# Kernel optimization log

Hardware: AMD Instinct MI355X
Metric: run time of the kernel (lower is better)

Reference implementation:

```python
import jax, jax.numpy as jnp
import numpy as np

B, S, D, F, E = 4, 2048, 512, 2048, 8


def setup_inputs() -> dict:
    key = jax.random.key(0)
    ks = jax.random.split(key, 8)
    s1 = 1.0 / np.sqrt(D)
    s2 = 1.0 / np.sqrt(F)
    return {
        "hidden_states": jax.random.normal(ks[0], (B, S, D), jnp.float32),
        "gating_probs": jax.random.uniform(ks[1], (B, S, E), jnp.float32),
        "shared_gate_prob": jax.random.uniform(ks[2], (B, S, 1), jnp.float32),
        "W1": jax.random.normal(ks[3], (E, D, F), jnp.float32) * s1,
        "b1": jnp.zeros((E, F), jnp.float32),
        "W2": jax.random.normal(ks[4], (E, F, D), jnp.float32) * s2,
        "b2": jnp.zeros((E, D), jnp.float32),
        "Ws1": jax.random.normal(ks[5], (D, F), jnp.float32) * s1,
        "bs1": jnp.zeros((F,), jnp.float32),
        "Ws2": jax.random.normal(ks[6], (F, D), jnp.float32) * s2,
        "bs2": jnp.zeros((D,), jnp.float32),
    }


def reference(hidden_states, gating_probs, shared_gate_prob,
              W1, b1, W2, b2, Ws1, bs1, Ws2, bs2):
    # Dense evaluation of ALL experts over all tokens (faithful to the source).
    # h: [B, E, S, F]
    h = jax.nn.gelu(jnp.einsum("bsd,edf->besf", hidden_states, W1) + b1[None, :, None, :])
    # y: [B, E, S, D]
    y = jnp.einsum("besf,efd->besd", h, W2) + b2[None, :, None, :]
    # weighted_sum combine with per-token gating probs: [B, S, D]
    expert_output = jnp.einsum("besd,bse->bsd", y, gating_probs)
    # shared expert
    hs = jax.nn.gelu(hidden_states @ Ws1 + bs1)
    shared_out = hs @ Ws2 + bs2
    return (1.0 - shared_gate_prob) * expert_output + shared_gate_prob * shared_out
```

## Files before the change

### kernel.cpp

```cpp
#include <hip/hip_runtime.h>

#define Dm 512
#define Fm 2048
#define Mm 8192
#define KTOT 18432

typedef __attribute__((ext_vector_type(8))) short short8;
typedef __attribute__((ext_vector_type(4))) float f32x4;


__device__ __forceinline__ unsigned short f2bf(float f) {
  unsigned u = __builtin_bit_cast(unsigned, f);
  u = (u + 0x7FFFu + ((u >> 16) & 1u)) >> 16;
  return (unsigned short)u;
}

__device__ __forceinline__ float fast_exp2(float x) {
  float r; asm("v_exp_f32 %0, %1" : "=v"(r) : "v"(x)); return r;
}
__device__ __forceinline__ float fast_rcp(float x) {
  float r; asm("v_rcp_f32 %0, %1" : "=v"(r) : "v"(x)); return r;
}

__device__ __forceinline__ void gload_lds16(const void* g, void* lp) {
  __builtin_amdgcn_global_load_lds(
      (const __attribute__((address_space(1))) void*)(unsigned long long)(g),
      (__attribute__((address_space(3))) void*)(unsigned)(unsigned long long)(lp),
      16, 0, 0);
}

__device__ __forceinline__ f32x4 mfma16(short8 a, short8 b, f32x4 c) {
  asm("v_mfma_f32_16x16x32_bf16 %0, %1, %2, %0" : "+v"(c) : "v"(a), "v"(b));
  return c;
}

#define WAIT_BARRIER(n) asm volatile("s_waitcnt vmcnt(" #n ")\n\ts_barrier" ::: "memory")


__global__ void cvtx_k(const float* __restrict__ src, unsigned short* __restrict__ dst, int n) {
  int i = (blockIdx.x * 256 + threadIdx.x) * 4;
  if (i >= n) return;
  const float4 v = *(const float4*)(src + i);
  unsigned a = (unsigned)f2bf(v.x) | ((unsigned)f2bf(v.y) << 16);
  unsigned b = (unsigned)f2bf(v.z) | ((unsigned)f2bf(v.w) << 16);
  uint2 o; o.x = a; o.y = b;
  *(uint2*)(dst + i) = o;
}

__global__ void wts_k(const float* __restrict__ gp, const float* __restrict__ sg,
                      float* __restrict__ wts) {
  int t = blockIdx.x * 256 + threadIdx.x;
  if (t >= Mm) return;
  float s = sg[t];
  float om = 1.0f - s;
#pragma unroll
  for (int e = 0; e < 8; ++e) wts[t * 9 + e] = om * gp[t * 8 + e];
  wts[t * 9 + 8] = s;
}

__global__ void wt_k(const float* __restrict__ W1, const float* __restrict__ Ws1,
                     const float* __restrict__ W2, const float* __restrict__ Ws2,
                     unsigned short* __restrict__ W1T, unsigned short* __restrict__ W2T) {
  __shared__ float tile[32][33];
  const int tx = threadIdx.x, ty = threadIdx.y;
  int bid = blockIdx.x;
  if (bid < 9216) {
    const int e = bid >> 10;
    const int rem = bid & 1023;
    const float* src = (e < 8) ? (W1 + (size_t)e * Dm * Fm) : Ws1;
    const int c0 = (rem & 63) << 5;
    const int r0 = (rem >> 6) << 5;
#pragma unroll
    for (int j = ty; j < 32; j += 8) tile[j][tx] = src[(size_t)(r0 + j) * Fm + c0 + tx];
    __syncthreads();
    unsigned short* de = W1T + (size_t)e * Fm * Dm;
#pragma unroll
    for (int j = ty; j < 32; j += 8) de[(size_t)(c0 + j) * Dm + r0 + tx] = f2bf(tile[tx][j]);
  } else {
    bid -= 9216;
    const int e = bid >> 10;
    const int rem = bid & 1023;
    const float* src = (e < 8) ? (W2 + (size_t)e * Fm * Dm) : Ws2;
    const int c0 = (rem & 15) << 5;
    const int r0 = (rem >> 4) << 5;
#pragma unroll
    for (int j = ty; j < 32; j += 8) tile[j][tx] = src[(size_t)(r0 + j) * Dm + c0 + tx];
    __syncthreads();
#pragma unroll
    for (int j = ty; j < 32; j += 8)
      W2T[(size_t)(c0 + j) * KTOT + (size_t)e * Fm + r0 + tx] = f2bf(tile[tx][j]);
  }
}


__global__ __launch_bounds__(256)
void gemm1_k(const unsigned short* __restrict__ Xb,
             const unsigned short* __restrict__ W1T,
             const float* __restrict__ b1, const float* __restrict__ bs1,
             const float* __restrict__ wts,
             unsigned short* __restrict__ Hs,
             int gbase, int Gg, int ldH) {
  __shared__ __attribute__((aligned(16))) unsigned short As[2][128 * 64];
  __shared__ __attribute__((aligned(16))) unsigned short Bs[2][128 * 64];

  const int tid = threadIdx.x, l = tid & 63, w = tid >> 6;
  const int wr = w >> 1, wc = w & 1;
  const int nwg = Gg << 10;
  const int wg = (blockIdx.x & 7) * (nwg >> 3) + (blockIdx.x >> 3);
  const int el = wg >> 10;
  const int rem = wg & 1023;
  const int grp = rem >> 7;
  const int sub = rem & 127;
  const int tn = (sub & 15) << 7;
  const int tm = ((grp << 3) + (sub >> 4)) << 7;
  const int eg = gbase + el;
  const unsigned short* BT = W1T + (size_t)eg * Fm * Dm;
  const float* bias = (eg < 8) ? (b1 + (size_t)eg * Fm) : bs1;

  f32x4 acc[4][4];
  const f32x4 zz = {0.f, 0.f, 0.f, 0.f};
#pragma unroll
  for (int mi = 0; mi < 4; ++mi)
#pragma unroll
    for (int ni = 0; ni < 4; ++ni) acc[mi][ni] = zz;

  const int srow = tid >> 3;
  const int sc = ((tid & 7) ^ (srow & 7)) << 3;

#define BPERM1(r) (((r) & 64) | (((r) & 15) << 2) | (((r) >> 4) & 3))

#define STAGE1(buf, ks)                                                          \
  {                                                                              \
    _Pragma("unroll")                                                            \
    for (int i = 0; i < 4; ++i) {                                                \
      const int row = i * 32 + srow;                                             \
      gload_lds16(Xb + (size_t)(tm + row) * Dm + (ks) + sc,                      \
                  (char*)As[buf] + i * 4096 + tid * 16);                         \
      gload_lds16(BT + (size_t)(tn + BPERM1(row)) * Dm + (ks) + sc,              \
                  (char*)Bs[buf] + i * 4096 + tid * 16);                         \
    }                                                                            \
  }

  STAGE1(0, 0);
  __syncthreads();

  for (int t = 0; t < 8; ++t) {
    const int cur = t & 1;
    if (t < 7) STAGE1(cur ^ 1, (t + 1) << 6);
#pragma unroll
    for (int kk = 0; kk < 2; ++kk) {
      const int kbx = (kk * 64 + ((l >> 4) << 4)) ^ ((l & 7) << 4);
      short8 af[4], bfr[4];
#pragma unroll
      for (int mi = 0; mi < 4; ++mi)
        af[mi] = *(const short8*)((const char*)As[cur] + ((wr * 64 + mi * 16 + (l & 15)) << 7) + kbx);
#pragma unroll
      for (int ni = 0; ni < 4; ++ni)
        bfr[ni] = *(const short8*)((const char*)Bs[cur] + ((wc * 64 + ni * 16 + (l & 15)) << 7) + kbx);
#pragma unroll
      for (int mi = 0; mi < 4; ++mi)
#pragma unroll
        for (int ni = 0; ni < 4; ++ni)
          acc[mi][ni] = mfma16(af[mi], bfr[ni], acc[mi][ni]);
    }
    if (t < 7) __syncthreads();
  }
#undef STAGE1
#undef BPERM1

  const int row0 = tm + wr * 64 + ((l >> 4) << 2);
  const int col0 = tn + wc * 64 + ((l & 15) << 2);
  const size_t hb = (size_t)el * Fm;
  const float4 bv = *(const float4*)(bias + col0);

  const float Ac = -2.3022120f;
  const float Bc = -0.10294341f;

#pragma unroll
  for (int mi = 0; mi < 4; ++mi) {
#pragma unroll
    for (int r = 0; r < 4; ++r) {
      const int rr = row0 + mi * 16 + r;
      const float wt = wts[(size_t)rr * 9 + eg];
      float g[4];
      const float bvv[4] = {bv.x, bv.y, bv.z, bv.w};
#pragma unroll
      for (int ni = 0; ni < 4; ++ni) {
        const float v = acc[mi][ni][r] + bvv[ni];
        const float t2 = v * fmaf(Bc, v * v, Ac);
        g[ni] = wt * v * fast_rcp(1.0f + fast_exp2(t2));
      }
      uint2 pk;
      asm("v_cvt_pk_bf16_f32 %0, %1, %2" : "=v"(pk.x) : "v"(g[0]), "v"(g[1]));
      asm("v_cvt_pk_bf16_f32 %0, %1, %2" : "=v"(pk.y) : "v"(g[2]), "v"(g[3]));
      *(uint2*)(Hs + (size_t)rr * ldH + hb + col0) = pk;
    }
  }
}


__global__ __launch_bounds__(256)
void gemm2_k(const unsigned short* __restrict__ A, int lda,
             const unsigned short* __restrict__ BT, int ldb,
             float* __restrict__ out,
             const float* __restrict__ wts,
             const float* __restrict__ b2, const float* __restrict__ bs2,
             int Kt, int g0) {
  __shared__ __attribute__((aligned(16))) unsigned short As[3][128 * 64];
  __shared__ __attribute__((aligned(16))) unsigned short Bs[3][64 * 64];

  const int tid = threadIdx.x, l = tid & 63, w = tid >> 6;
  const int wr = w >> 1, wc = w & 1;
  const int wg = (blockIdx.x & 7) * 64 + (blockIdx.x >> 3);
  const int gm = wg >> 6;
  const int sub = wg & 63;
  const int tn = (sub & 7) << 6;
  const int tm = ((gm << 3) + (sub >> 3)) << 7;

  f32x4 acc[4][2];
  const f32x4 zz = {0.f, 0.f, 0.f, 0.f};
#pragma unroll
  for (int mi = 0; mi < 4; ++mi)
#pragma unroll
    for (int ni = 0; ni < 2; ++ni) acc[mi][ni] = zz;

  const int srow = tid >> 3;
  const int sc = ((tid & 7) ^ (srow & 7)) << 3;

#define BPERM2(r) (((r) & 32) | (((r) & 15) << 1) | (((r) >> 4) & 1))

#define STAGE2(buf, ks)                                                          \
  {                                                                              \
    _Pragma("unroll")                                                            \
    for (int i = 0; i < 4; ++i) {                                                \
      const int row = i * 32 + srow;                                             \
      gload_lds16(A + (size_t)(tm + row) * lda + (ks) + sc,                      \
                  (char*)As[buf] + i * 4096 + tid * 16);                         \
    }                                                                            \
    _Pragma("unroll")                                                            \
    for (int i = 0; i < 2; ++i) {                                                \
      const int row = i * 32 + srow;                                             \
      gload_lds16(BT + (size_t)(tn + BPERM2(row)) * ldb + (ks) + sc,             \
                  (char*)Bs[buf] + i * 4096 + tid * 16);                         \
    }                                                                            \
  }

  const int NT = Kt >> 6;
  STAGE2(0, 0);
  STAGE2(1, 64);

#pragma unroll 1
  for (int t = 0; t < NT; ++t) {
    const int cur = t % 3;
    if (t + 1 < NT) { WAIT_BARRIER(6); }
    else            { WAIT_BARRIER(0); }
    __builtin_amdgcn_sched_barrier(0);
    if (t + 2 < NT) {
      const int nb = (t + 2) % 3;
      STAGE2(nb, (t + 2) << 6);
    }
#pragma unroll
    for (int kk = 0; kk < 2; ++kk) {
      const int kbx = (kk * 64 + ((l >> 4) << 4)) ^ ((l & 7) << 4);
      short8 af[4], bfr[2];
#pragma unroll
      for (int mi = 0; mi < 4; ++mi)
        af[mi] = *(const short8*)((const char*)As[cur] + ((wr * 64 + mi * 16 + (l & 15)) << 7) + kbx);
#pragma unroll
      for (int ni = 0; ni < 2; ++ni)
        bfr[ni] = *(const short8*)((const char*)Bs[cur] + ((wc * 32 + ni * 16 + (l & 15)) << 7) + kbx);
#pragma unroll
      for (int mi = 0; mi < 4; ++mi)
#pragma unroll
        for (int ni = 0; ni < 2; ++ni)
          acc[mi][ni] = mfma16(af[mi], bfr[ni], acc[mi][ni]);
    }
  }
#undef STAGE2
#undef BPERM2

  const int row0 = tm + wr * 64 + ((l >> 4) << 2);
  const int col0 = tn + wc * 32 + ((l & 15) << 1);

  if (g0) {
    float bcol[2][9];
#pragma unroll
    for (int ni = 0; ni < 2; ++ni) {
      const int c = col0 + ni;
#pragma unroll
      for (int e = 0; e < 8; ++e) bcol[ni][e] = b2[(e << 9) + c];
      bcol[ni][8] = bs2[c];
    }
#pragma unroll
    for (int mi = 0; mi < 4; ++mi)
#pragma unroll
      for (int r = 0; r < 4; ++r) {
        const int rr = row0 + mi * 16 + r;
        const float* wrow = wts + (size_t)rr * 9;
        float b0 = 0.f, b1v = 0.f;
#pragma unroll
        for (int e = 0; e < 9; ++e) { b0 += wrow[e] * bcol[0][e]; b1v += wrow[e] * bcol[1][e]; }
        float2 o;
        o.x = acc[mi][0][r] + b0;
        o.y = acc[mi][1][r] + b1v;
        *(float2*)(out + (size_t)rr * Dm + col0) = o;
      }
  } else {
#pragma unroll
    for (int mi = 0; mi < 4; ++mi)
#pragma unroll
      for (int r = 0; r < 4; ++r) {
        float* p = out + (size_t)(row0 + mi * 16 + r) * Dm + col0;
        float2 o = *(float2*)p;
        o.x += acc[mi][0][r];
        o.y += acc[mi][1][r];
        *(float2*)p = o;
      }
  }
}


extern "C" void kernel_launch(void* const* d_in, const int* in_sizes, int n_in,
                              void* d_out, int out_size, void* d_ws, size_t ws_size,
                              hipStream_t stream) {
  const float* x   = (const float*)d_in[0];
  const float* gp  = (const float*)d_in[1];
  const float* sg  = (const float*)d_in[2];
  const float* W1  = (const float*)d_in[3];
  const float* b1  = (const float*)d_in[4];
  const float* W2  = (const float*)d_in[5];
  const float* b2  = (const float*)d_in[6];
  const float* Ws1 = (const float*)d_in[7];
  const float* bs1 = (const float*)d_in[8];
  const float* Ws2 = (const float*)d_in[9];
  const float* bs2 = (const float*)d_in[10];
  float* out = (float*)d_out;

  const size_t szXb  = (size_t)Mm * Dm * 2;
  const size_t szWts = (size_t)Mm * 9 * 4;
  const size_t szW1T = (size_t)9 * Fm * Dm * 2;
  const size_t szW2T = (size_t)9 * Fm * Dm * 2;
  const size_t base  = szXb + szWts + szW1T + szW2T;

  int G;
  if      (ws_size >= base + (size_t)Mm * 9 * Fm * 2) G = 9;
  else if (ws_size >= base + (size_t)Mm * 3 * Fm * 2) G = 3;
  else if (ws_size >= base + (size_t)Mm * 2 * Fm * 2) G = 2;
  else if (ws_size >= base + (size_t)Mm * 1 * Fm * 2) G = 1;
  else return;

  char* ws = (char*)d_ws;
  unsigned short* Xb  = (unsigned short*)(ws);
  float*          wts = (float*)(ws + szXb);
  unsigned short* W1T = (unsigned short*)(ws + szXb + szWts);
  unsigned short* W2T = (unsigned short*)(ws + szXb + szWts + szW1T);
  unsigned short* Hs  = (unsigned short*)(ws + base);
  const int ldH = G * Fm;

  cvtx_k<<<dim3((Mm * Dm) / 1024), dim3(256), 0, stream>>>(x, Xb, Mm * Dm);
  wts_k<<<dim3(Mm / 256), dim3(256), 0, stream>>>(gp, sg, wts);
  wt_k<<<dim3(2 * 9 * 1024), dim3(32, 8), 0, stream>>>(W1, Ws1, W2, Ws2, W1T, W2T);

  for (int gb = 0; gb < 9; gb += G) {
    const int Gg = (9 - gb < G) ? (9 - gb) : G;
    gemm1_k<<<dim3(Gg * 1024), dim3(256), 0, stream>>>(
        Xb, W1T, b1, bs1, wts, Hs, gb, Gg, ldH);
    gemm2_k<<<dim3(512), dim3(256), 0, stream>>>(
        Hs, ldH, W2T + (size_t)gb * Fm, KTOT, out, wts, b2, bs2, Gg * Fm, gb == 0 ? 1 : 0);
  }
}
```

Baseline: 422.0 us.

## Make gemm1 persistent with 128x64 tiles and a triple-buffered continuous pipeline

gemm1 now launches a fixed 512 workgroups. Each one walks a sequence of 128x64 output tiles and keeps a three-stage LDS pipeline running across tile boundaries, using vmcnt-based waits in place of full syncthreads. Gating weights are written in an expert-major copy so the epilogue can read them as vectors. The aim is to hide load latency and remove per-tile launch and drain costs, at the price of smaller tiles that reuse less data and an extra workspace buffer.

```diff
diff --git a/kernel.cpp b/kernel.cpp
--- a/kernel.cpp
+++ b/kernel.cpp
@@ -35,6 +35,8 @@
 }
 
 #define WAIT_BARRIER(n) asm volatile("s_waitcnt vmcnt(" #n ")\n\ts_barrier" ::: "memory")
+
+#define BPERM2(r) (((r) & 32) | (((r) & 15) << 1) | (((r) >> 4) & 1))
 
 
 __global__ void cvtx_k(const float* __restrict__ src, unsigned short* __restrict__ dst, int n) {
@@ -48,14 +50,19 @@
 }
 
 __global__ void wts_k(const float* __restrict__ gp, const float* __restrict__ sg,
-                      float* __restrict__ wts) {
+                      float* __restrict__ wts, float* __restrict__ wtsE) {
   int t = blockIdx.x * 256 + threadIdx.x;
   if (t >= Mm) return;
   float s = sg[t];
   float om = 1.0f - s;
 #pragma unroll
-  for (int e = 0; e < 8; ++e) wts[t * 9 + e] = om * gp[t * 8 + e];
+  for (int e = 0; e < 8; ++e) {
+    float v = om * gp[t * 8 + e];
+    wts[t * 9 + e] = v;
+    wtsE[(size_t)e * Mm + t] = v;
+  }
   wts[t * 9 + 8] = s;
+  wtsE[(size_t)8 * Mm + t] = s;
 }
 
 __global__ void wt_k(const float* __restrict__ W1, const float* __restrict__ Ws1,
@@ -97,105 +104,130 @@
 void gemm1_k(const unsigned short* __restrict__ Xb,
              const unsigned short* __restrict__ W1T,
              const float* __restrict__ b1, const float* __restrict__ bs1,
-             const float* __restrict__ wts,
+             const float* __restrict__ wtsE,
              unsigned short* __restrict__ Hs,
              int gbase, int Gg, int ldH) {
-  __shared__ __attribute__((aligned(16))) unsigned short As[2][128 * 64];
-  __shared__ __attribute__((aligned(16))) unsigned short Bs[2][128 * 64];
+  __shared__ __attribute__((aligned(16))) unsigned short As[3][128 * 64];
+  __shared__ __attribute__((aligned(16))) unsigned short Bs[3][64 * 64];
 
   const int tid = threadIdx.x, l = tid & 63, w = tid >> 6;
   const int wr = w >> 1, wc = w & 1;
-  const int nwg = Gg << 10;
-  const int wg = (blockIdx.x & 7) * (nwg >> 3) + (blockIdx.x >> 3);
-  const int el = wg >> 10;
-  const int rem = wg & 1023;
-  const int grp = rem >> 7;
-  const int sub = rem & 127;
-  const int tn = (sub & 15) << 7;
-  const int tm = ((grp << 3) + (sub >> 4)) << 7;
-  const int eg = gbase + el;
-  const unsigned short* BT = W1T + (size_t)eg * Fm * Dm;
-  const float* bias = (eg < 8) ? (b1 + (size_t)eg * Fm) : bs1;
-
-  f32x4 acc[4][4];
+  const int TPB = Gg << 2;
+  const int NS = TPB << 3;
+  const int cbase = ((blockIdx.x & 7) * 64 + (blockIdx.x >> 3)) * TPB;
+
+  f32x4 acc[4][2];
   const f32x4 zz = {0.f, 0.f, 0.f, 0.f};
 #pragma unroll
   for (int mi = 0; mi < 4; ++mi)
 #pragma unroll
-    for (int ni = 0; ni < 4; ++ni) acc[mi][ni] = zz;
+    for (int ni = 0; ni < 2; ++ni) acc[mi][ni] = zz;
 
   const int srow = tid >> 3;
   const int sc = ((tid & 7) ^ (srow & 7)) << 3;
 
-#define BPERM1(r) (((r) & 64) | (((r) & 15) << 2) | (((r) >> 4) & 3))
-
-#define STAGE1(buf, ks)                                                          \
+#define STAGEP(buf, s2)                                                          \
   {                                                                              \
+    const int T_ = cbase + ((s2) >> 3);                                          \
+    const int e_ = T_ >> 11;                                                     \
+    const int rem_ = T_ & 2047;                                                  \
+    const int tn_ = (rem_ & 31) << 6;                                            \
+    const int tm_ = (rem_ >> 5) << 7;                                            \
+    const int ks_ = ((s2) & 7) << 6;                                             \
+    const unsigned short* BT_ = W1T + (size_t)(gbase + e_) * (Fm * Dm);          \
     _Pragma("unroll")                                                            \
     for (int i = 0; i < 4; ++i) {                                                \
       const int row = i * 32 + srow;                                             \
-      gload_lds16(Xb + (size_t)(tm + row) * Dm + (ks) + sc,                      \
+      gload_lds16(Xb + (size_t)(tm_ + row) * Dm + ks_ + sc,                      \
                   (char*)As[buf] + i * 4096 + tid * 16);                         \
-      gload_lds16(BT + (size_t)(tn + BPERM1(row)) * Dm + (ks) + sc,              \
+    }                                                                            \
+    _Pragma("unroll")                                                            \
+    for (int i = 0; i < 2; ++i) {                                                \
+      const int row = i * 32 + srow;                                             \
+      gload_lds16(BT_ + (size_t)(tn_ + BPERM2(row)) * Dm + ks_ + sc,             \
                   (char*)Bs[buf] + i * 4096 + tid * 16);                         \
     }                                                                            \
   }
 
-  STAGE1(0, 0);
-  __syncthreads();
-
-  for (int t = 0; t < 8; ++t) {
-    const int cur = t & 1;
-    if (t < 7) STAGE1(cur ^ 1, (t + 1) << 6);
-#pragma unroll
-    for (int kk = 0; kk < 2; ++kk) {
-      const int kbx = (kk * 64 + ((l >> 4) << 4)) ^ ((l & 7) << 4);
-      short8 af[4], bfr[4];
-#pragma unroll
-      for (int mi = 0; mi < 4; ++mi)
-        af[mi] = *(const short8*)((const char*)As[cur] + ((wr * 64 + mi * 16 + (l & 15)) << 7) + kbx);
-#pragma unroll
-      for (int ni = 0; ni < 4; ++ni)
-        bfr[ni] = *(const short8*)((const char*)Bs[cur] + ((wc * 64 + ni * 16 + (l & 15)) << 7) + kbx);
-#pragma unroll
-      for (int mi = 0; mi < 4; ++mi)
-#pragma unroll
-        for (int ni = 0; ni < 4; ++ni)
-          acc[mi][ni] = mfma16(af[mi], bfr[ni], acc[mi][ni]);
-    }
-    if (t < 7) __syncthreads();
-  }
-#undef STAGE1
-#undef BPERM1
-
-  const int row0 = tm + wr * 64 + ((l >> 4) << 2);
-  const int col0 = tn + wc * 64 + ((l & 15) << 2);
-  const size_t hb = (size_t)el * Fm;
-  const float4 bv = *(const float4*)(bias + col0);
+  STAGEP(0, 0);
+  STAGEP(1, 1);
 
   const float Ac = -2.3022120f;
   const float Bc = -0.10294341f;
 
-#pragma unroll
-  for (int mi = 0; mi < 4; ++mi) {
-#pragma unroll
-    for (int r = 0; r < 4; ++r) {
-      const int rr = row0 + mi * 16 + r;
-      const float wt = wts[(size_t)rr * 9 + eg];
-      float g[4];
-      const float bvv[4] = {bv.x, bv.y, bv.z, bv.w};
-#pragma unroll
-      for (int ni = 0; ni < 4; ++ni) {
-        const float v = acc[mi][ni][r] + bvv[ni];
-        const float t2 = v * fmaf(Bc, v * v, Ac);
-        g[ni] = wt * v * fast_rcp(1.0f + fast_exp2(t2));
+  int cur = 0;
+#pragma unroll 1
+  for (int j = 0; j < TPB; ++j) {
+    const int T = cbase + j;
+    const int el = T >> 11;
+    const int eg = gbase + el;
+    const int rem = T & 2047;
+    const int tnj = (rem & 31) << 6;
+    const int tmj = (rem >> 5) << 7;
+    const float* bias = (eg < 8) ? (b1 + (size_t)eg * Fm) : bs1;
+    const int row0 = tmj + wr * 64 + ((l >> 4) << 2);
+    const int col0 = tnj + wc * 32 + ((l & 15) << 1);
+    f32x4 wq[4];
+#pragma unroll
+    for (int mi = 0; mi < 4; ++mi)
+      wq[mi] = *(const f32x4*)(wtsE + (size_t)eg * Mm + row0 + mi * 16);
+    const float2 bv = *(const float2*)(bias + col0);
+
+#pragma unroll 1
+    for (int t = 0; t < 8; ++t) {
+      const int s = (j << 3) + t;
+      if (s + 1 < NS) { WAIT_BARRIER(6); } else { WAIT_BARRIER(0); }
+      __builtin_amdgcn_sched_barrier(0);
+      if (s + 2 < NS) {
+        int nb = cur + 2; if (nb >= 3) nb -= 3;
+        STAGEP(nb, s + 2);
       }
-      uint2 pk;
-      asm("v_cvt_pk_bf16_f32 %0, %1, %2" : "=v"(pk.x) : "v"(g[0]), "v"(g[1]));
-      asm("v_cvt_pk_bf16_f32 %0, %1, %2" : "=v"(pk.y) : "v"(g[2]), "v"(g[3]));
-      *(uint2*)(Hs + (size_t)rr * ldH + hb + col0) = pk;
+#pragma unroll
+      for (int kk = 0; kk < 2; ++kk) {
+        const int kbx = (kk * 64 + ((l >> 4) << 4)) ^ ((l & 7) << 4);
+        short8 af[4], bfr[2];
+#pragma unroll
+        for (int mi = 0; mi < 4; ++mi)
+          af[mi] = *(const short8*)((const char*)As[cur] + ((wr * 64 + mi * 16 + (l & 15)) << 7) + kbx);
+#pragma unroll
+        for (int ni = 0; ni < 2; ++ni)
+          bfr[ni] = *(const short8*)((const char*)Bs[cur] + ((wc * 32 + ni * 16 + (l & 15)) << 7) + kbx);
+#pragma unroll
+        for (int mi = 0; mi < 4; ++mi)
+#pragma unroll
+          for (int ni = 0; ni < 2; ++ni)
+            acc[mi][ni] = mfma16(af[mi], bfr[ni], acc[mi][ni]);
+      }
+      cur = (cur + 1 == 3) ? 0 : cur + 1;
     }
-  }
+
+    const size_t hb = (size_t)el * Fm;
+#pragma unroll
+    for (int mi = 0; mi < 4; ++mi) {
+#pragma unroll
+      for (int r = 0; r < 4; ++r) {
+        const int rr = row0 + mi * 16 + r;
+        const float wt = wq[mi][r];
+        float g0, g1;
+        {
+          const float v = acc[mi][0][r] + bv.x;
+          const float t2 = v * fmaf(Bc, v * v, Ac);
+          g0 = wt * v * fast_rcp(1.0f + fast_exp2(t2));
+        }
+        {
+          const float v = acc[mi][1][r] + bv.y;
+          const float t2 = v * fmaf(Bc, v * v, Ac);
+          g1 = wt * v * fast_rcp(1.0f + fast_exp2(t2));
+        }
+        unsigned pk;
+        asm("v_cvt_pk_bf16_f32 %0, %1, %2" : "=v"(pk) : "v"(g0), "v"(g1));
+        *(unsigned*)(Hs + (size_t)rr * ldH + hb + col0) = pk;
+        acc[mi][0][r] = 0.f;
+        acc[mi][1][r] = 0.f;
+      }
+    }
+  }
+#undef STAGEP
 }
 
 
@@ -226,8 +258,6 @@
 
   const int srow = tid >> 3;
   const int sc = ((tid & 7) ^ (srow & 7)) << 3;
-
-#define BPERM2(r) (((r) & 32) | (((r) & 15) << 1) | (((r) >> 4) & 1))
 
 #define STAGE2(buf, ks)                                                          \
   {                                                                              \
@@ -277,7 +307,6 @@
     }
   }
 #undef STAGE2
-#undef BPERM2
 
   const int row0 = tm + wr * 64 + ((l >> 4) << 2);
   const int col0 = tn + wc * 32 + ((l & 15) << 1);
@@ -336,11 +365,12 @@
   const float* bs2 = (const float*)d_in[10];
   float* out = (float*)d_out;
 
-  const size_t szXb  = (size_t)Mm * Dm * 2;
-  const size_t szWts = (size_t)Mm * 9 * 4;
-  const size_t szW1T = (size_t)9 * Fm * Dm * 2;
-  const size_t szW2T = (size_t)9 * Fm * Dm * 2;
-  const size_t base  = szXb + szWts + szW1T + szW2T;
+  const size_t szXb   = (size_t)Mm * Dm * 2;
+  const size_t szWts  = (size_t)Mm * 9 * 4;
+  const size_t szWtsE = (size_t)Mm * 9 * 4;
+  const size_t szW1T  = (size_t)9 * Fm * Dm * 2;
+  const size_t szW2T  = (size_t)9 * Fm * Dm * 2;
+  const size_t base   = szXb + szWts + szWtsE + szW1T + szW2T;
 
   int G;
   if      (ws_size >= base + (size_t)Mm * 9 * Fm * 2) G = 9;
@@ -350,21 +380,22 @@
   else return;
 
   char* ws = (char*)d_ws;
-  unsigned short* Xb  = (unsigned short*)(ws);
-  float*          wts = (float*)(ws + szXb);
-  unsigned short* W1T = (unsigned short*)(ws + szXb + szWts);
-  unsigned short* W2T = (unsigned short*)(ws + szXb + szWts + szW1T);
-  unsigned short* Hs  = (unsigned short*)(ws + base);
+  unsigned short* Xb   = (unsigned short*)(ws);
+  float*          wts  = (float*)(ws + szXb);
+  float*          wtsE = (float*)(ws + szXb + szWts);
+  unsigned short* W1T  = (unsigned short*)(ws + szXb + szWts + szWtsE);
+  unsigned short* W2T  = (unsigned short*)(ws + szXb + szWts + szWtsE + szW1T);
+  unsigned short* Hs   = (unsigned short*)(ws + base);
   const int ldH = G * Fm;
 
   cvtx_k<<<dim3((Mm * Dm) / 1024), dim3(256), 0, stream>>>(x, Xb, Mm * Dm);
-  wts_k<<<dim3(Mm / 256), dim3(256), 0, stream>>>(gp, sg, wts);
+  wts_k<<<dim3(Mm / 256), dim3(256), 0, stream>>>(gp, sg, wts, wtsE);
   wt_k<<<dim3(2 * 9 * 1024), dim3(32, 8), 0, stream>>>(W1, Ws1, W2, Ws2, W1T, W2T);
 
   for (int gb = 0; gb < 9; gb += G) {
     const int Gg = (9 - gb < G) ? (9 - gb) : G;
-    gemm1_k<<<dim3(Gg * 1024), dim3(256), 0, stream>>>(
-        Xb, W1T, b1, bs1, wts, Hs, gb, Gg, ldH);
+    gemm1_k<<<dim3(512), dim3(256), 0, stream>>>(
+        Xb, W1T, b1, bs1, wtsE, Hs, gb, Gg, ldH);
     gemm2_k<<<dim3(512), dim3(256), 0, stream>>>(
         Hs, ldH, W2T + (size_t)gb * Fm, KTOT, out, wts, b2, bs2, Gg * Fm, gb == 0 ? 1 : 0);
   }
```

Measured after the change: 485.8 us. +15.1%, slower.

## Use four-stage K=32 LDS pipeline in gemm1 with vmcnt waits and setprio

Applied to the files above, without the earlier changes.

Replaces gemm1's double-buffered K=64 tile loop with a four-slot ring of K=32 tiles that are prefetched two steps ahead. Each step uses a single vmcnt-based wait plus barrier and raises wave priority around the MFMA block. The aim is to keep more global-to-LDS loads in flight and hide load latency behind matrix math. In exchange there are twice as many barriers per K, a different LDS swizzle, and the correctness of the slot reuse depends on those wait counts.

```diff
diff --git a/kernel.cpp b/kernel.cpp
--- a/kernel.cpp
+++ b/kernel.cpp
@@ -35,6 +35,10 @@
 }
 
 #define WAIT_BARRIER(n) asm volatile("s_waitcnt vmcnt(" #n ")\n\ts_barrier" ::: "memory")
+
+#define BPERM1(r) (((r) & 64) | (((r) & 15) << 2) | (((r) >> 4) & 3))
+
+#define BPERM2(r) (((r) & 32) | (((r) & 15) << 1) | (((r) >> 4) & 1))
 
 
 __global__ void cvtx_k(const float* __restrict__ src, unsigned short* __restrict__ dst, int n) {
@@ -100,8 +104,8 @@
              const float* __restrict__ wts,
              unsigned short* __restrict__ Hs,
              int gbase, int Gg, int ldH) {
-  __shared__ __attribute__((aligned(16))) unsigned short As[2][128 * 64];
-  __shared__ __attribute__((aligned(16))) unsigned short Bs[2][128 * 64];
+  __shared__ __attribute__((aligned(16))) unsigned short As[4][128 * 32];
+  __shared__ __attribute__((aligned(16))) unsigned short Bs[4][128 * 32];
 
   const int tid = threadIdx.x, l = tid & 63, w = tid >> 6;
   const int wr = w >> 1, wc = w & 1;
@@ -124,49 +128,56 @@
 #pragma unroll
     for (int ni = 0; ni < 4; ++ni) acc[mi][ni] = zz;
 
-  const int srow = tid >> 3;
-  const int sc = ((tid & 7) ^ (srow & 7)) << 3;
-
-#define BPERM1(r) (((r) & 64) | (((r) & 15) << 2) | (((r) >> 4) & 3))
-
-#define STAGE1(buf, ks)                                                          \
-  {                                                                              \
-    _Pragma("unroll")                                                            \
-    for (int i = 0; i < 4; ++i) {                                                \
-      const int row = i * 32 + srow;                                             \
-      gload_lds16(Xb + (size_t)(tm + row) * Dm + (ks) + sc,                      \
-                  (char*)As[buf] + i * 4096 + tid * 16);                         \
-      gload_lds16(BT + (size_t)(tn + BPERM1(row)) * Dm + (ks) + sc,              \
-                  (char*)Bs[buf] + i * 4096 + tid * 16);                         \
-    }                                                                            \
+  const int srowL = tid >> 2;
+  const int selem = ((tid & 3) ^ (srowL & 3)) << 3;
+
+#define STAGE1(slot, p2)                                                        \
+  {                                                                             \
+    const int ks_ = (p2) << 5;                                                  \
+    _Pragma("unroll")                                                           \
+    for (int i = 0; i < 2; ++i) {                                               \
+      const int R = i * 64 + srowL;                                             \
+      gload_lds16(Xb + (size_t)(tm + R) * Dm + ks_ + selem,                     \
+                  (char*)As[slot] + i * 4096 + tid * 16);                       \
+      gload_lds16(BT + (size_t)(tn + BPERM1(R)) * Dm + ks_ + selem,             \
+                  (char*)Bs[slot] + i * 4096 + tid * 16);                       \
+    }                                                                           \
   }
 
   STAGE1(0, 0);
-  __syncthreads();
-
-  for (int t = 0; t < 8; ++t) {
-    const int cur = t & 1;
-    if (t < 7) STAGE1(cur ^ 1, (t + 1) << 6);
-#pragma unroll
-    for (int kk = 0; kk < 2; ++kk) {
-      const int kbx = (kk * 64 + ((l >> 4) << 4)) ^ ((l & 7) << 4);
-      short8 af[4], bfr[4];
-#pragma unroll
-      for (int mi = 0; mi < 4; ++mi)
-        af[mi] = *(const short8*)((const char*)As[cur] + ((wr * 64 + mi * 16 + (l & 15)) << 7) + kbx);
+  STAGE1(1, 1);
+
+  const int kby = (((l >> 4) ^ (l & 3)) << 4);
+  const int arow = ((wr << 6) + (l & 15)) << 6;
+  const int brow = ((wc << 6) + (l & 15)) << 6;
+
+#pragma unroll 1
+  for (int p = 0; p < 16; ++p) {
+    if (p < 15) { WAIT_BARRIER(4); }
+    else        { WAIT_BARRIER(0); }
+    __builtin_amdgcn_sched_barrier(0);
+    if (p < 14) {
+      const int slot = (p + 2) & 3;
+      STAGE1(slot, p + 2);
+    }
+    const char* Ab = (const char*)As[p & 3];
+    const char* Bb = (const char*)Bs[p & 3];
+    short8 af[4], bfr[4];
+#pragma unroll
+    for (int mi = 0; mi < 4; ++mi)
+      af[mi] = *(const short8*)(Ab + arow + (mi << 10) + kby);
+#pragma unroll
+    for (int ni = 0; ni < 4; ++ni)
+      bfr[ni] = *(const short8*)(Bb + brow + (ni << 10) + kby);
+    __builtin_amdgcn_s_setprio(1);
+#pragma unroll
+    for (int mi = 0; mi < 4; ++mi)
 #pragma unroll
       for (int ni = 0; ni < 4; ++ni)
-        bfr[ni] = *(const short8*)((const char*)Bs[cur] + ((wc * 64 + ni * 16 + (l & 15)) << 7) + kbx);
-#pragma unroll
-      for (int mi = 0; mi < 4; ++mi)
-#pragma unroll
-        for (int ni = 0; ni < 4; ++ni)
-          acc[mi][ni] = mfma16(af[mi], bfr[ni], acc[mi][ni]);
-    }
-    if (t < 7) __syncthreads();
+        acc[mi][ni] = mfma16(af[mi], bfr[ni], acc[mi][ni]);
+    __builtin_amdgcn_s_setprio(0);
   }
 #undef STAGE1
-#undef BPERM1
 
   const int row0 = tm + wr * 64 + ((l >> 4) << 2);
   const int col0 = tn + wc * 64 + ((l & 15) << 2);
@@ -226,8 +237,6 @@
 
   const int srow = tid >> 3;
   const int sc = ((tid & 7) ^ (srow & 7)) << 3;
-
-#define BPERM2(r) (((r) & 32) | (((r) & 15) << 1) | (((r) >> 4) & 1))
 
 #define STAGE2(buf, ks)                                                          \
   {                                                                              \
@@ -277,7 +286,6 @@
     }
   }
 #undef STAGE2
-#undef BPERM2
 
   const int row0 = tm + wr * 64 + ((l >> 4) << 2);
   const int col0 = tn + wc * 32 + ((l & 15) << 1);
```

Measured after the change: 443.5 us. 5.1% more time.

## Overlap gemm2 of previous expert group with gemm1 of next group in one launch

Applied to the files above, without the earlier changes.

Merges the two GEMM kernels into a single kernel whose blocks run either the up-projection for group i or the down-projection for group i-1. Hs is double-buffered so the two stages can run concurrently, and gemm2 blocks are interleaved with gemm1 blocks to fill the GPU. This removes the tail and launch gaps between dependent launches. In exchange the shared LDS footprint grows to 72KB, which can cut occupancy for the gemm1 path, and G is capped at 3, which adds launches compared with G=9.

```diff
diff --git a/kernel.cpp b/kernel.cpp
--- a/kernel.cpp
+++ b/kernel.cpp
@@ -35,6 +35,9 @@
 }
 
 #define WAIT_BARRIER(n) asm volatile("s_waitcnt vmcnt(" #n ")\n\ts_barrier" ::: "memory")
+
+#define BPERM1(r) (((r) & 64) | (((r) & 15) << 2) | (((r) >> 4) & 3))
+#define BPERM2(r) (((r) & 32) | (((r) & 15) << 1) | (((r) >> 4) & 1))
 
 
 __global__ void cvtx_k(const float* __restrict__ src, unsigned short* __restrict__ dst, int n) {
@@ -93,20 +96,21 @@
 }
 
 
-__global__ __launch_bounds__(256)
-void gemm1_k(const unsigned short* __restrict__ Xb,
-             const unsigned short* __restrict__ W1T,
-             const float* __restrict__ b1, const float* __restrict__ bs1,
-             const float* __restrict__ wts,
-             unsigned short* __restrict__ Hs,
-             int gbase, int Gg, int ldH) {
-  __shared__ __attribute__((aligned(16))) unsigned short As[2][128 * 64];
-  __shared__ __attribute__((aligned(16))) unsigned short Bs[2][128 * 64];
+__device__ __forceinline__ void gemm1_body(
+    int v, char* smem,
+    const unsigned short* __restrict__ Xb,
+    const unsigned short* __restrict__ W1T,
+    const float* __restrict__ b1, const float* __restrict__ bs1,
+    const float* __restrict__ wts,
+    unsigned short* __restrict__ Hs,
+    int gbase, int Gg, int ldH) {
+  char* AsB = smem;
+  char* BsB = smem + 32768;
 
   const int tid = threadIdx.x, l = tid & 63, w = tid >> 6;
   const int wr = w >> 1, wc = w & 1;
   const int nwg = Gg << 10;
-  const int wg = (blockIdx.x & 7) * (nwg >> 3) + (blockIdx.x >> 3);
+  const int wg = (v & 7) * (nwg >> 3) + (v >> 3);
   const int el = wg >> 10;
   const int rem = wg & 1023;
   const int grp = rem >> 7;
@@ -127,17 +131,15 @@
   const int srow = tid >> 3;
   const int sc = ((tid & 7) ^ (srow & 7)) << 3;
 
-#define BPERM1(r) (((r) & 64) | (((r) & 15) << 2) | (((r) >> 4) & 3))
-
 #define STAGE1(buf, ks)                                                          \
   {                                                                              \
     _Pragma("unroll")                                                            \
     for (int i = 0; i < 4; ++i) {                                                \
       const int row = i * 32 + srow;                                             \
       gload_lds16(Xb + (size_t)(tm + row) * Dm + (ks) + sc,                      \
-                  (char*)As[buf] + i * 4096 + tid * 16);                         \
+                  AsB + (buf) * 16384 + i * 4096 + tid * 16);                    \
       gload_lds16(BT + (size_t)(tn + BPERM1(row)) * Dm + (ks) + sc,              \
-                  (char*)Bs[buf] + i * 4096 + tid * 16);                         \
+                  BsB + (buf) * 16384 + i * 4096 + tid * 16);                    \
     }                                                                            \
   }
 
@@ -153,10 +155,10 @@
       short8 af[4], bfr[4];
 #pragma unroll
       for (int mi = 0; mi < 4; ++mi)
-        af[mi] = *(const short8*)((const char*)As[cur] + ((wr * 64 + mi * 16 + (l & 15)) << 7) + kbx);
+        af[mi] = *(const short8*)(AsB + cur * 16384 + ((wr * 64 + mi * 16 + (l & 15)) << 7) + kbx);
 #pragma unroll
       for (int ni = 0; ni < 4; ++ni)
-        bfr[ni] = *(const short8*)((const char*)Bs[cur] + ((wc * 64 + ni * 16 + (l & 15)) << 7) + kbx);
+        bfr[ni] = *(const short8*)(BsB + cur * 16384 + ((wc * 64 + ni * 16 + (l & 15)) << 7) + kbx);
 #pragma unroll
       for (int mi = 0; mi < 4; ++mi)
 #pragma unroll
@@ -166,7 +168,6 @@
     if (t < 7) __syncthreads();
   }
 #undef STAGE1
-#undef BPERM1
 
   const int row0 = tm + wr * 64 + ((l >> 4) << 2);
   const int col0 = tn + wc * 64 + ((l & 15) << 2);
@@ -186,9 +187,9 @@
       const float bvv[4] = {bv.x, bv.y, bv.z, bv.w};
 #pragma unroll
       for (int ni = 0; ni < 4; ++ni) {
-        const float v = acc[mi][ni][r] + bvv[ni];
-        const float t2 = v * fmaf(Bc, v * v, Ac);
-        g[ni] = wt * v * fast_rcp(1.0f + fast_exp2(t2));
+        const float vv = acc[mi][ni][r] + bvv[ni];
+        const float t2 = vv * fmaf(Bc, vv * vv, Ac);
+        g[ni] = wt * vv * fast_rcp(1.0f + fast_exp2(t2));
       }
       uint2 pk;
       asm("v_cvt_pk_bf16_f32 %0, %1, %2" : "=v"(pk.x) : "v"(g[0]), "v"(g[1]));
@@ -199,19 +200,20 @@
 }
 
 
-__global__ __launch_bounds__(256)
-void gemm2_k(const unsigned short* __restrict__ A, int lda,
-             const unsigned short* __restrict__ BT, int ldb,
-             float* __restrict__ out,
-             const float* __restrict__ wts,
-             const float* __restrict__ b2, const float* __restrict__ bs2,
-             int Kt, int g0) {
-  __shared__ __attribute__((aligned(16))) unsigned short As[3][128 * 64];
-  __shared__ __attribute__((aligned(16))) unsigned short Bs[3][64 * 64];
+__device__ __forceinline__ void gemm2_body(
+    int v, char* smem,
+    const unsigned short* __restrict__ A, int lda,
+    const unsigned short* __restrict__ BT, int ldb,
+    float* __restrict__ out,
+    const float* __restrict__ wts,
+    const float* __restrict__ b2, const float* __restrict__ bs2,
+    int Kt, int g0) {
+  char* AsB = smem;
+  char* BsB = smem + 49152;
 
   const int tid = threadIdx.x, l = tid & 63, w = tid >> 6;
   const int wr = w >> 1, wc = w & 1;
-  const int wg = (blockIdx.x & 7) * 64 + (blockIdx.x >> 3);
+  const int wg = (v & 7) * 64 + (v >> 3);
   const int gm = wg >> 6;
   const int sub = wg & 63;
   const int tn = (sub & 7) << 6;
@@ -226,8 +228,6 @@
 
   const int srow = tid >> 3;
   const int sc = ((tid & 7) ^ (srow & 7)) << 3;
-
-#define BPERM2(r) (((r) & 32) | (((r) & 15) << 1) | (((r) >> 4) & 1))
 
 #define STAGE2(buf, ks)                                                          \
   {                                                                              \
@@ -235,13 +235,13 @@
     for (int i = 0; i < 4; ++i) {                                                \
       const int row = i * 32 + srow;                                             \
       gload_lds16(A + (size_t)(tm + row) * lda + (ks) + sc,                      \
-                  (char*)As[buf] + i * 4096 + tid * 16);                         \
+                  AsB + (buf) * 16384 + i * 4096 + tid * 16);                    \
     }                                                                            \
     _Pragma("unroll")                                                            \
     for (int i = 0; i < 2; ++i) {                                                \
       const int row = i * 32 + srow;                                             \
       gload_lds16(BT + (size_t)(tn + BPERM2(row)) * ldb + (ks) + sc,             \
-                  (char*)Bs[buf] + i * 4096 + tid * 16);                         \
+                  BsB + (buf) * 8192 + i * 4096 + tid * 16);                     \
     }                                                                            \
   }
 
@@ -265,10 +265,10 @@
       short8 af[4], bfr[2];
 #pragma unroll
       for (int mi = 0; mi < 4; ++mi)
-        af[mi] = *(const short8*)((const char*)As[cur] + ((wr * 64 + mi * 16 + (l & 15)) << 7) + kbx);
+        af[mi] = *(const short8*)(AsB + cur * 16384 + ((wr * 64 + mi * 16 + (l & 15)) << 7) + kbx);
 #pragma unroll
       for (int ni = 0; ni < 2; ++ni)
-        bfr[ni] = *(const short8*)((const char*)Bs[cur] + ((wc * 32 + ni * 16 + (l & 15)) << 7) + kbx);
+        bfr[ni] = *(const short8*)(BsB + cur * 8192 + ((wc * 32 + ni * 16 + (l & 15)) << 7) + kbx);
 #pragma unroll
       for (int mi = 0; mi < 4; ++mi)
 #pragma unroll
@@ -277,7 +277,6 @@
     }
   }
 #undef STAGE2
-#undef BPERM2
 
   const int row0 = tm + wr * 64 + ((l >> 4) << 2);
   const int col0 = tn + wc * 32 + ((l & 15) << 1);
@@ -316,6 +315,38 @@
         o.y += acc[mi][1][r];
         *(float2*)p = o;
       }
+  }
+}
+
+
+__global__ __launch_bounds__(256)
+void moe_k(const unsigned short* __restrict__ Xb,
+           const unsigned short* __restrict__ W1T,
+           const float* __restrict__ b1, const float* __restrict__ bs1,
+           const float* __restrict__ wts,
+           unsigned short* __restrict__ Hs1,
+           int gbase1, int Gg1, int ldH,
+           const unsigned short* __restrict__ Hs2,
+           const unsigned short* __restrict__ BT2,
+           float* __restrict__ out,
+           const float* __restrict__ b2, const float* __restrict__ bs2,
+           int Kt2, int g0, int n1, int has2) {
+  __shared__ __attribute__((aligned(16))) char smem[73728];
+  if (!has2) {
+    gemm1_body(blockIdx.x, smem, Xb, W1T, b1, bs1, wts, Hs1, gbase1, Gg1, ldH);
+    return;
+  }
+  if (n1 == 0) {
+    gemm2_body(blockIdx.x, smem, Hs2, ldH, BT2, KTOT, out, wts, b2, bs2, Kt2, g0);
+    return;
+  }
+  const int R = (n1 >> 9) + 1;
+  const int bid = blockIdx.x;
+  const int q = bid / R;
+  if (bid - q * R == 0) {
+    gemm2_body(q, smem, Hs2, ldH, BT2, KTOT, out, wts, b2, bs2, Kt2, g0);
+  } else {
+    gemm1_body(bid - q - 1, smem, Xb, W1T, b1, bs1, wts, Hs1, gbase1, Gg1, ldH);
   }
 }
 
@@ -343,10 +374,9 @@
   const size_t base  = szXb + szWts + szW1T + szW2T;
 
   int G;
-  if      (ws_size >= base + (size_t)Mm * 9 * Fm * 2) G = 9;
-  else if (ws_size >= base + (size_t)Mm * 3 * Fm * 2) G = 3;
-  else if (ws_size >= base + (size_t)Mm * 2 * Fm * 2) G = 2;
-  else if (ws_size >= base + (size_t)Mm * 1 * Fm * 2) G = 1;
+  if      (ws_size >= base + 2 * (size_t)Mm * 3 * Fm * 2) G = 3;
+  else if (ws_size >= base + 2 * (size_t)Mm * 2 * Fm * 2) G = 2;
+  else if (ws_size >= base + 2 * (size_t)Mm * 1 * Fm * 2) G = 1;
   else return;
 
   char* ws = (char*)d_ws;
@@ -354,18 +384,40 @@
   float*          wts = (float*)(ws + szXb);
   unsigned short* W1T = (unsigned short*)(ws + szXb + szWts);
   unsigned short* W2T = (unsigned short*)(ws + szXb + szWts + szW1T);
-  unsigned short* Hs  = (unsigned short*)(ws + base);
+  const size_t szHs = (size_t)Mm * G * Fm * 2;
+  unsigned short* HsA = (unsigned short*)(ws + base);
+  unsigned short* HsB = (unsigned short*)(ws + base + szHs);
   const int ldH = G * Fm;
 
   cvtx_k<<<dim3((Mm * Dm) / 1024), dim3(256), 0, stream>>>(x, Xb, Mm * Dm);
   wts_k<<<dim3(Mm / 256), dim3(256), 0, stream>>>(gp, sg, wts);
   wt_k<<<dim3(2 * 9 * 1024), dim3(32, 8), 0, stream>>>(W1, Ws1, W2, Ws2, W1T, W2T);
 
-  for (int gb = 0; gb < 9; gb += G) {
-    const int Gg = (9 - gb < G) ? (9 - gb) : G;
-    gemm1_k<<<dim3(Gg * 1024), dim3(256), 0, stream>>>(
-        Xb, W1T, b1, bs1, wts, Hs, gb, Gg, ldH);
-    gemm2_k<<<dim3(512), dim3(256), 0, stream>>>(
-        Hs, ldH, W2T + (size_t)gb * Fm, KTOT, out, wts, b2, bs2, Gg * Fm, gb == 0 ? 1 : 0);
-  }
-}
+  const int nG = (9 + G - 1) / G;
+  for (int i = 0; i <= nG; ++i) {
+    const int gb1 = i * G;
+    const int Gg1 = (i < nG) ? ((9 - gb1 < G) ? 9 - gb1 : G) : 0;
+    const int gb2 = (i - 1) * G;
+    const int Gg2 = (i > 0) ? ((9 - gb2 < G) ? 9 - gb2 : G) : 0;
+    unsigned short* Hs1 = (i & 1) ? HsB : HsA;
+    unsigned short* Hs2 = ((i - 1) & 1) ? HsB : HsA;
+
+    if (i == 0) {
+      const int n1 = Gg1 << 10;
+      moe_k<<<dim3(n1), dim3(256), 0, stream>>>(
+          Xb, W1T, b1, bs1, wts, Hs1, gb1, Gg1, ldH,
+          HsA, W2T, out, b2, bs2, 0, 0, n1, 0);
+    } else if (i == nG) {
+      moe_k<<<dim3(512), dim3(256), 0, stream>>>(
+          Xb, W1T, b1, bs1, wts, Hs1, 0, 1, ldH,
+          Hs2, W2T + (size_t)gb2 * Fm, out, b2, bs2, Gg2 * Fm, (gb2 == 0) ? 1 : 0,
+          0, 1);
+    } else {
+      const int n1 = Gg1 << 10;
+      moe_k<<<dim3(n1 + 512), dim3(256), 0, stream>>>(
+          Xb, W1T, b1, bs1, wts, Hs1, gb1, Gg1, ldH,
+          Hs2, W2T + (size_t)gb2 * Fm, out, b2, bs2, Gg2 * Fm, (gb2 == 0) ? 1 : 0,
+          n1, 1);
+    }
+  }
+}
```

Result: slower. 602.0 us (+42.7%).
